# Optimization experiments

Measured on AMD Instinct MI355X. Metric: run time of the kernel, lower is better.

The kernel has to match this reference:

```python
import jax, jax.numpy as jnp
import numpy as np

ALPHA = 0.5
SIGMA = 0.5
EPS = 1e-7

def setup_inputs() -> dict:
    key = jax.random.key(0)
    k1, k2, k3, k4 = jax.random.split(key, 4)
    n, T = 8192, 256
    return {
        "hazards": jax.random.normal(k1, (n, T), dtype=jnp.float32),
        "duration": jax.random.randint(k2, (n,), 0, T, dtype=jnp.int32),
        "event": jax.random.randint(k3, (n,), 0, 2, dtype=jnp.int32),
        "label": jax.random.randint(k4, (n,), 0, T, dtype=jnp.int32),
    }

def _deephit_loss(hazards, duration, event, label):
    dur = duration.reshape(-1)
    ev = event.reshape(-1)
    lab = label.reshape(-1)
    evf = ev.astype(hazards.dtype)

    # pair_rank_mat: R_ij = 1{D_i=1 and (T_i < T_j or (T_i == T_j and D_j = 0))}
    rank_mat = ((ev[:, None] != 0)
                & ((dur[:, None] < dur[None, :])
                   | ((dur[:, None] == dur[None, :]) & (ev[None, :] == 0)))
                ).astype(hazards.dtype)  # [n, n]

    # nll_pmf (pad_col adds a zero column -> T+1 bins)
    phi = jnp.pad(hazards, ((0, 0), (0, 1)))            # [n, T+1]
    gamma = jnp.max(phi, axis=1)                         # [n]
    cumsum = jnp.cumsum(jnp.exp(phi - gamma[:, None]), axis=1)  # [n, T+1]
    sum_ = cumsum[:, -1]
    phi_at = jnp.take_along_axis(phi, lab[:, None], axis=1)[:, 0]
    cum_at = jnp.take_along_axis(cumsum, lab[:, None], axis=1)[:, 0]
    part1 = (phi_at - gamma) * evf
    part2 = -jnp.log(jnp.maximum(sum_, 0.0) + EPS)
    part3 = jnp.log(jnp.maximum(sum_ - cum_at, 0.0) + EPS) * (1.0 - evf)
    nll = jnp.mean(-(part1 + part2 + part3))

    # rank_loss_deephit_single
    pmf = jax.nn.softmax(phi, axis=1)                    # [n, T+1]
    cdf = jnp.cumsum(pmf, axis=1)                        # [n, T+1]
    y = jax.nn.one_hot(lab, phi.shape[1], dtype=pmf.dtype)  # [n, T+1]
    r = cdf @ y.T                                        # r_ij = F_i(T_j), [n, n]
    diag_r = jnp.diagonal(r)                             # F_j(T_j)
    r = (diag_r[None, :] - r).T                          # r_ij = F_i(T_i) - F_j(T_i)
    rank_loss = jnp.mean(rank_mat * jnp.exp(-r / SIGMA))

    return ALPHA * nll + (1.0 - ALPHA) * rank_loss

def reference(hazards, duration, event, label):
    return _deephit_loss(hazards, duration, event, label)
```

## Files before the change

kernel.cpp:

```cpp
#include <hip/hip_runtime.h>
#include <hip/hip_fp16.h>

#define TBINS 256
#define RPB   16
#define NTHR  1024
#define EPS_F 1e-7f
#define INV_SIGMA 2.0f

__global__ __launch_bounds__(NTHR) void row_kernel(
    const float* __restrict__ hz, const int* __restrict__ dur,
    const int* __restrict__ ev,  const int* __restrict__ lab,
    __half* __restrict__ WT, float* __restrict__ rowA,
    float* __restrict__ nllpart, int n)
{
    __shared__ float trs[RPB][260];
    __shared__ float nllred[RPB];

    const int wid  = threadIdx.x >> 6;
    const int lane = threadIdx.x & 63;
    const int row  = blockIdx.x * RPB + wid;
    const bool act = row < n;
    const int rrow = act ? row : 0;

    const float4 v = ((const float4*)(hz + (size_t)rrow * TBINS))[lane];

    float m = fmaxf(fmaxf(v.x, v.y), fmaxf(v.z, v.w));
    #pragma unroll
    for (int off = 32; off; off >>= 1) m = fmaxf(m, __shfl_xor(m, off));
    const float gamma = fmaxf(m, 0.0f);

    const float e0 = expf(v.x - gamma), e1 = expf(v.y - gamma);
    const float e2 = expf(v.z - gamma), e3 = expf(v.w - gamma);
    const float local = e0 + e1 + e2 + e3;

    float pre = local;
    #pragma unroll
    for (int off = 1; off < 64; off <<= 1) {
        float tv = __shfl_up(pre, off);
        if (lane >= off) pre += tv;
    }
    const float excl  = pre - local;
    const float total = __shfl(pre, 63);
    const float sum_  = total + expf(-gamma);
    const float c0 = excl + e0, c1 = c0 + e1, c2 = c1 + e2, c3 = c2 + e3;

    const int L = lab[rrow];
    const int e = ev[rrow];
    const int sel = L & 3;
    float csel = (sel == 0) ? c0 : (sel == 1) ? c1 : (sel == 2) ? c2 : c3;
    const float cum_at = __shfl(csel, L >> 2);
    const float inv = 1.0f / sum_;

    float4 w;
    w.x = expf(c0 * inv * INV_SIGMA);
    w.y = expf(c1 * inv * INV_SIGMA);
    w.z = expf(c2 * inv * INV_SIGMA);
    w.w = expf(c3 * inv * INV_SIGMA);
    *(float4*)&trs[wid][4 * lane] = w;

    if (lane == 0) {
        float nll_i = 0.f, a_i = 0.f;
        if (act) {
            const float phi_at = hz[(size_t)row * TBINS + L];
            const float evf = (float)e;
            const float p1 = (phi_at - gamma) * evf;
            const float p2 = -logf(fmaxf(sum_, 0.f) + EPS_F);
            const float p3 = logf(fmaxf(sum_ - cum_at, 0.f) + EPS_F) * (1.f - evf);
            nll_i = -(p1 + p2 + p3);
            a_i = e ? expf(-(cum_at * inv) * INV_SIGMA) : 0.f;
            rowA[row] = a_i;
        }
        nllred[wid] = nll_i;
    }
    __syncthreads();

    if (threadIdx.x == 0) {
        float s = 0.f;
        #pragma unroll
        for (int k = 0; k < RPB; ++k) s += nllred[k];
        nllpart[blockIdx.x] = s;
    }

    const int t  = threadIdx.x >> 2;
    const int j  = threadIdx.x & 3;
    const int i0 = blockIdx.x * RPB + 4 * j;
    if (i0 + 3 < n) {
        ushort4 p;
        p.x = __half_as_ushort(__float2half(trs[4 * j + 0][t]));
        p.y = __half_as_ushort(__float2half(trs[4 * j + 1][t]));
        p.z = __half_as_ushort(__float2half(trs[4 * j + 2][t]));
        p.w = __half_as_ushort(__float2half(trs[4 * j + 3][t]));
        *(ushort4*)&WT[(size_t)t * n + i0] = p;
    }
}

__global__ __launch_bounds__(NTHR) void agg_kernel(
    const __half* __restrict__ WT, const int* __restrict__ dur,
    const int* __restrict__ ev, float* __restrict__ B, int n)
{
    __shared__ float bins[512];

    const int t   = blockIdx.x;
    const int tid = threadIdx.x;

    if (tid < 512) bins[tid] = 0.f;
    __syncthreads();

    const __half* w = WT + (size_t)t * n;
    const int i0 = tid * 8;
    if (i0 + 7 < n) {
        const ushort4 ha = *(const ushort4*)&w[i0];
        const ushort4 hb = *(const ushort4*)&w[i0 + 4];
        const int4 da = *(const int4*)&dur[i0];
        const int4 db = *(const int4*)&dur[i0 + 4];
        const int4 ea = *(const int4*)&ev[i0];
        const int4 eb = *(const int4*)&ev[i0 + 4];
        atomicAdd(&bins[da.x + (ea.x << 8)], __half2float(__ushort_as_half(ha.x)));
        atomicAdd(&bins[da.y + (ea.y << 8)], __half2float(__ushort_as_half(ha.y)));
        atomicAdd(&bins[da.z + (ea.z << 8)], __half2float(__ushort_as_half(ha.z)));
        atomicAdd(&bins[da.w + (ea.w << 8)], __half2float(__ushort_as_half(ha.w)));
        atomicAdd(&bins[db.x + (eb.x << 8)], __half2float(__ushort_as_half(hb.x)));
        atomicAdd(&bins[db.y + (eb.y << 8)], __half2float(__ushort_as_half(hb.y)));
        atomicAdd(&bins[db.z + (eb.z << 8)], __half2float(__ushort_as_half(hb.z)));
        atomicAdd(&bins[db.w + (eb.w << 8)], __half2float(__ushort_as_half(hb.w)));
    }
    __syncthreads();

    if (tid < 64) {
        const int d0 = tid * 4;
        const float g0 = bins[d0 + 0] + bins[d0 + 256];
        const float g1 = bins[d0 + 1] + bins[d0 + 257];
        const float g2 = bins[d0 + 2] + bins[d0 + 258];
        const float g3 = bins[d0 + 3] + bins[d0 + 259];
        const float c0 = g0, c1 = c0 + g1, c2 = c1 + g2, c3 = c2 + g3;
        float pre = c3;
        #pragma unroll
        for (int off = 1; off < 64; off <<= 1) {
            float tv = __shfl_up(pre, off);
            if (tid >= off) pre += tv;
        }
        const float excl  = pre - c3;
        const float tot   = __shfl(pre, 63);
        float4 ob;
        ob.x = (tot - (excl + c0)) + bins[d0 + 0];
        ob.y = (tot - (excl + c1)) + bins[d0 + 1];
        ob.z = (tot - (excl + c2)) + bins[d0 + 2];
        ob.w = (tot - (excl + c3)) + bins[d0 + 3];
        *(float4*)&B[t * TBINS + d0] = ob;
    }
}

__global__ __launch_bounds__(NTHR) void rank_final_kernel(
    const int* __restrict__ dur, const int* __restrict__ lab,
    const float* __restrict__ rowA, const float* __restrict__ B,
    const float* __restrict__ nllpart, float* __restrict__ out,
    int n, int nblk)
{
    const int tid  = threadIdx.x;
    const int wid  = tid >> 6;
    const int lane = tid & 63;
    __shared__ float rs[16], ss[16];

    float r = 0.f;
    for (int i = tid; i < n; i += NTHR) {
        const float a = rowA[i];
        if (a != 0.f) r += a * B[lab[i] * TBINS + dur[i]];
    }
    float s = (tid < nblk) ? nllpart[tid] : 0.f;

    #pragma unroll
    for (int off = 32; off; off >>= 1) {
        r += __shfl_xor(r, off);
        s += __shfl_xor(s, off);
    }
    if (lane == 0) { rs[wid] = r; ss[wid] = s; }
    __syncthreads();
    if (tid == 0) {
        float R = 0.f, S = 0.f;
        #pragma unroll
        for (int k = 0; k < 16; ++k) { R += rs[k]; S += ss[k]; }
        const double nll = (double)S / (double)n;
        const double rl  = (double)R / ((double)n * (double)n);
        out[0] = (float)(0.5 * nll + 0.5 * rl);
    }
}

extern "C" void kernel_launch(void* const* d_in, const int* in_sizes, int n_in,
                              void* d_out, int out_size, void* d_ws, size_t ws_size,
                              hipStream_t stream) {
    const float* hz  = (const float*)d_in[0];
    const int*   dur = (const int*)d_in[1];
    const int*   ev  = (const int*)d_in[2];
    const int*   lab = (const int*)d_in[3];
    float* out = (float*)d_out;

    const int n = in_sizes[1];
    const int nblk = (n + RPB - 1) / RPB;

    __half* WT     = (__half*)d_ws;
    float*  B      = (float*)(WT + (size_t)TBINS * n);
    float*  rowA   = B + TBINS * TBINS;
    float*  nllpart= rowA + n;

    row_kernel<<<nblk, NTHR, 0, stream>>>(hz, dur, ev, lab, WT, rowA, nllpart, n);
    agg_kernel<<<TBINS, NTHR, 0, stream>>>(WT, dur, ev, B, n);
    rank_final_kernel<<<1, NTHR, 0, stream>>>(dur, lab, rowA, B, nllpart, out, n, nblk);
}
```

Before: 89.84 us.

## Fuse rank aggregation and final reduction into histogram kernel with last-block finish

The separate single-block final kernel is folded into the histogram kernel. Each block computes its own B row in shared memory and sums contributions from rows whose label matches its bin, then a global atomic counter lets the last block finish the reduction. The histogram is split into per-wave copies to reduce shared atomic contention, and the row kernel now handles two rows per wave. This removes a launch and the serial single-block pass, in exchange for global atomics, an order-dependent float sum, and a threadfence handshake.

```diff
diff --git a/kernel.cpp b/kernel.cpp
--- a/kernel.cpp
+++ b/kernel.cpp
@@ -2,136 +2,168 @@
 #include <hip/hip_fp16.h>
 
 #define TBINS 256
-#define RPB   16
+#define RPB   32
 #define NTHR  1024
 #define EPS_F 1e-7f
 #define INV_SIGMA 2.0f
 
 __global__ __launch_bounds__(NTHR) void row_kernel(
-    const float* __restrict__ hz, const int* __restrict__ dur,
-    const int* __restrict__ ev,  const int* __restrict__ lab,
+    const float* __restrict__ hz, const int* __restrict__ ev,
+    const int* __restrict__ lab,
     __half* __restrict__ WT, float* __restrict__ rowA,
-    float* __restrict__ nllpart, int n)
+    float* __restrict__ nllpart, float* __restrict__ accR, int* __restrict__ done,
+    int n)
 {
-    __shared__ float trs[RPB][260];
+    __shared__ float trs[RPB][261];
     __shared__ float nllred[RPB];
 
-    const int wid  = threadIdx.x >> 6;
-    const int lane = threadIdx.x & 63;
-    const int row  = blockIdx.x * RPB + wid;
-    const bool act = row < n;
-    const int rrow = act ? row : 0;
-
-    const float4 v = ((const float4*)(hz + (size_t)rrow * TBINS))[lane];
-
-    float m = fmaxf(fmaxf(v.x, v.y), fmaxf(v.z, v.w));
+    const int tid  = threadIdx.x;
+    const int wid  = tid >> 6;
+    const int lane = tid & 63;
+
+    if (blockIdx.x == 0 && tid == 0) { *accR = 0.f; *done = 0; }
+
     #pragma unroll
-    for (int off = 32; off; off >>= 1) m = fmaxf(m, __shfl_xor(m, off));
-    const float gamma = fmaxf(m, 0.0f);
-
-    const float e0 = expf(v.x - gamma), e1 = expf(v.y - gamma);
-    const float e2 = expf(v.z - gamma), e3 = expf(v.w - gamma);
-    const float local = e0 + e1 + e2 + e3;
-
-    float pre = local;
-    #pragma unroll
-    for (int off = 1; off < 64; off <<= 1) {
-        float tv = __shfl_up(pre, off);
-        if (lane >= off) pre += tv;
-    }
-    const float excl  = pre - local;
-    const float total = __shfl(pre, 63);
-    const float sum_  = total + expf(-gamma);
-    const float c0 = excl + e0, c1 = c0 + e1, c2 = c1 + e2, c3 = c2 + e3;
-
-    const int L = lab[rrow];
-    const int e = ev[rrow];
-    const int sel = L & 3;
-    float csel = (sel == 0) ? c0 : (sel == 1) ? c1 : (sel == 2) ? c2 : c3;
-    const float cum_at = __shfl(csel, L >> 2);
-    const float inv = 1.0f / sum_;
-
-    float4 w;
-    w.x = expf(c0 * inv * INV_SIGMA);
-    w.y = expf(c1 * inv * INV_SIGMA);
-    w.z = expf(c2 * inv * INV_SIGMA);
-    w.w = expf(c3 * inv * INV_SIGMA);
-    *(float4*)&trs[wid][4 * lane] = w;
-
-    if (lane == 0) {
-        float nll_i = 0.f, a_i = 0.f;
-        if (act) {
-            const float phi_at = hz[(size_t)row * TBINS + L];
-            const float evf = (float)e;
-            const float p1 = (phi_at - gamma) * evf;
-            const float p2 = -logf(fmaxf(sum_, 0.f) + EPS_F);
-            const float p3 = logf(fmaxf(sum_ - cum_at, 0.f) + EPS_F) * (1.f - evf);
-            nll_i = -(p1 + p2 + p3);
-            a_i = e ? expf(-(cum_at * inv) * INV_SIGMA) : 0.f;
-            rowA[row] = a_i;
-        }
-        nllred[wid] = nll_i;
-    }
-    __syncthreads();
-
-    if (threadIdx.x == 0) {
+    for (int r = 0; r < 2; ++r) {
+        const int lrow = wid * 2 + r;
+        const int row  = blockIdx.x * RPB + lrow;
+        const bool act = row < n;
+        const int rrow = act ? row : 0;
+
+        const float4 v = ((const float4*)(hz + (size_t)rrow * TBINS))[lane];
+
+        float m = fmaxf(fmaxf(v.x, v.y), fmaxf(v.z, v.w));
+        #pragma unroll
+        for (int off = 32; off; off >>= 1) m = fmaxf(m, __shfl_xor(m, off));
+        const float gamma = fmaxf(m, 0.0f);
+
+        const float e0 = expf(v.x - gamma), e1 = expf(v.y - gamma);
+        const float e2 = expf(v.z - gamma), e3 = expf(v.w - gamma);
+        const float local = e0 + e1 + e2 + e3;
+
+        float pre = local;
+        #pragma unroll
+        for (int off = 1; off < 64; off <<= 1) {
+            float tv = __shfl_up(pre, off);
+            if (lane >= off) pre += tv;
+        }
+        const float excl  = pre - local;
+        const float total = __shfl(pre, 63);
+        const float sum_  = total + expf(-gamma);
+        const float c0 = excl + e0, c1 = c0 + e1, c2 = c1 + e2, c3 = c2 + e3;
+
+        const int L = lab[rrow];
+        const int e = ev[rrow];
+        const int sel = L & 3;
+        float csel = (sel == 0) ? c0 : (sel == 1) ? c1 : (sel == 2) ? c2 : c3;
+        const float cum_at = __shfl(csel, L >> 2);
+        const float inv = 1.0f / sum_;
+
+        float4 w;
+        w.x = expf(c0 * inv * INV_SIGMA);
+        w.y = expf(c1 * inv * INV_SIGMA);
+        w.z = expf(c2 * inv * INV_SIGMA);
+        w.w = expf(c3 * inv * INV_SIGMA);
+        *(float4*)&trs[lrow][4 * lane] = w;
+
+        if (lane == 0) {
+            float nll_i = 0.f, a_i = 0.f;
+            if (act) {
+                const float phi_at = hz[(size_t)row * TBINS + L];
+                const float evf = (float)e;
+                const float p1 = (phi_at - gamma) * evf;
+                const float p2 = -logf(fmaxf(sum_, 0.f) + EPS_F);
+                const float p3 = logf(fmaxf(sum_ - cum_at, 0.f) + EPS_F) * (1.f - evf);
+                nll_i = -(p1 + p2 + p3);
+                a_i = e ? expf(-(cum_at * inv) * INV_SIGMA) : 0.f;
+                rowA[row] = a_i;
+            }
+            nllred[lrow] = nll_i;
+        }
+    }
+    __syncthreads();
+
+    if (tid == 0) {
         float s = 0.f;
         #pragma unroll
         for (int k = 0; k < RPB; ++k) s += nllred[k];
         nllpart[blockIdx.x] = s;
     }
 
-    const int t  = threadIdx.x >> 2;
-    const int j  = threadIdx.x & 3;
-    const int i0 = blockIdx.x * RPB + 4 * j;
-    if (i0 + 3 < n) {
-        ushort4 p;
-        p.x = __half_as_ushort(__float2half(trs[4 * j + 0][t]));
-        p.y = __half_as_ushort(__float2half(trs[4 * j + 1][t]));
-        p.z = __half_as_ushort(__float2half(trs[4 * j + 2][t]));
-        p.w = __half_as_ushort(__float2half(trs[4 * j + 3][t]));
-        *(ushort4*)&WT[(size_t)t * n + i0] = p;
+    #pragma unroll
+    for (int k = 0; k < 2; ++k) {
+        const int t = (tid >> 3) + 128 * k;
+        const int j = tid & 7;
+        const int i0 = blockIdx.x * RPB + 4 * j;
+        if (i0 + 3 < n) {
+            ushort4 p;
+            p.x = __half_as_ushort(__float2half(trs[4 * j + 0][t]));
+            p.y = __half_as_ushort(__float2half(trs[4 * j + 1][t]));
+            p.z = __half_as_ushort(__float2half(trs[4 * j + 2][t]));
+            p.w = __half_as_ushort(__float2half(trs[4 * j + 3][t]));
+            *(ushort4*)&WT[(size_t)t * n + i0] = p;
+        }
     }
 }
 
-__global__ __launch_bounds__(NTHR) void agg_kernel(
+__global__ __launch_bounds__(NTHR) void agg_rank_kernel(
     const __half* __restrict__ WT, const int* __restrict__ dur,
-    const int* __restrict__ ev, float* __restrict__ B, int n)
+    const int* __restrict__ ev, const int* __restrict__ lab,
+    const float* __restrict__ rowA, const float* __restrict__ nllpart,
+    float* __restrict__ accR, int* __restrict__ done,
+    float* __restrict__ out, int n, int nblk1)
 {
-    __shared__ float bins[512];
-
-    const int t   = blockIdx.x;
-    const int tid = threadIdx.x;
-
-    if (tid < 512) bins[tid] = 0.f;
-    __syncthreads();
-
-    const __half* w = WT + (size_t)t * n;
-    const int i0 = tid * 8;
-    if (i0 + 7 < n) {
-        const ushort4 ha = *(const ushort4*)&w[i0];
-        const ushort4 hb = *(const ushort4*)&w[i0 + 4];
-        const int4 da = *(const int4*)&dur[i0];
-        const int4 db = *(const int4*)&dur[i0 + 4];
-        const int4 ea = *(const int4*)&ev[i0];
-        const int4 eb = *(const int4*)&ev[i0 + 4];
-        atomicAdd(&bins[da.x + (ea.x << 8)], __half2float(__ushort_as_half(ha.x)));
-        atomicAdd(&bins[da.y + (ea.y << 8)], __half2float(__ushort_as_half(ha.y)));
-        atomicAdd(&bins[da.z + (ea.z << 8)], __half2float(__ushort_as_half(ha.z)));
-        atomicAdd(&bins[da.w + (ea.w << 8)], __half2float(__ushort_as_half(ha.w)));
-        atomicAdd(&bins[db.x + (eb.x << 8)], __half2float(__ushort_as_half(hb.x)));
-        atomicAdd(&bins[db.y + (eb.y << 8)], __half2float(__ushort_as_half(hb.y)));
-        atomicAdd(&bins[db.z + (eb.z << 8)], __half2float(__ushort_as_half(hb.z)));
-        atomicAdd(&bins[db.w + (eb.w << 8)], __half2float(__ushort_as_half(hb.w)));
+    __shared__ float hist[16][512];
+    __shared__ float comb[512];
+    __shared__ float Brow[TBINS];
+    __shared__ float red[16];
+    __shared__ int lastflag;
+
+    const int t    = blockIdx.x;
+    const int tid  = threadIdx.x;
+    const int wid  = tid >> 6;
+    const int lane = tid & 63;
+
+    for (int i = tid; i < 16 * 512; i += NTHR) ((float*)hist)[i] = 0.f;
+    __syncthreads();
+
+    {
+        const __half* w = WT + (size_t)t * n;
+        const int i0 = tid * 8;
+        if (i0 + 7 < n) {
+            const ushort4 ha = *(const ushort4*)&w[i0];
+            const ushort4 hb = *(const ushort4*)&w[i0 + 4];
+            const int4 da = *(const int4*)&dur[i0];
+            const int4 db = *(const int4*)&dur[i0 + 4];
+            const int4 ea = *(const int4*)&ev[i0];
+            const int4 eb = *(const int4*)&ev[i0 + 4];
+            float* hb_ = hist[wid];
+            atomicAdd(&hb_[da.x + (ea.x << 8)], __half2float(__ushort_as_half(ha.x)));
+            atomicAdd(&hb_[da.y + (ea.y << 8)], __half2float(__ushort_as_half(ha.y)));
+            atomicAdd(&hb_[da.z + (ea.z << 8)], __half2float(__ushort_as_half(ha.z)));
+            atomicAdd(&hb_[da.w + (ea.w << 8)], __half2float(__ushort_as_half(ha.w)));
+            atomicAdd(&hb_[db.x + (eb.x << 8)], __half2float(__ushort_as_half(hb.x)));
+            atomicAdd(&hb_[db.y + (eb.y << 8)], __half2float(__ushort_as_half(hb.y)));
+            atomicAdd(&hb_[db.z + (eb.z << 8)], __half2float(__ushort_as_half(hb.z)));
+            atomicAdd(&hb_[db.w + (eb.w << 8)], __half2float(__ushort_as_half(hb.w)));
+        }
+    }
+    __syncthreads();
+
+    if (tid < 512) {
+        float s = 0.f;
+        #pragma unroll
+        for (int k = 0; k < 16; ++k) s += hist[k][tid];
+        comb[tid] = s;
     }
     __syncthreads();
 
     if (tid < 64) {
         const int d0 = tid * 4;
-        const float g0 = bins[d0 + 0] + bins[d0 + 256];
-        const float g1 = bins[d0 + 1] + bins[d0 + 257];
-        const float g2 = bins[d0 + 2] + bins[d0 + 258];
-        const float g3 = bins[d0 + 3] + bins[d0 + 259];
+        const float g0 = comb[d0 + 0] + comb[d0 + 256];
+        const float g1 = comb[d0 + 1] + comb[d0 + 257];
+        const float g2 = comb[d0 + 2] + comb[d0 + 258];
+        const float g3 = comb[d0 + 3] + comb[d0 + 259];
         const float c0 = g0, c1 = c0 + g1, c2 = c1 + g2, c3 = c2 + g3;
         float pre = c3;
         #pragma unroll
@@ -139,49 +171,63 @@
             float tv = __shfl_up(pre, off);
             if (tid >= off) pre += tv;
         }
-        const float excl  = pre - c3;
-        const float tot   = __shfl(pre, 63);
-        float4 ob;
-        ob.x = (tot - (excl + c0)) + bins[d0 + 0];
-        ob.y = (tot - (excl + c1)) + bins[d0 + 1];
-        ob.z = (tot - (excl + c2)) + bins[d0 + 2];
-        ob.w = (tot - (excl + c3)) + bins[d0 + 3];
-        *(float4*)&B[t * TBINS + d0] = ob;
-    }
-}
-
-__global__ __launch_bounds__(NTHR) void rank_final_kernel(
-    const int* __restrict__ dur, const int* __restrict__ lab,
-    const float* __restrict__ rowA, const float* __restrict__ B,
-    const float* __restrict__ nllpart, float* __restrict__ out,
-    int n, int nblk)
-{
-    const int tid  = threadIdx.x;
-    const int wid  = tid >> 6;
-    const int lane = tid & 63;
-    __shared__ float rs[16], ss[16];
-
-    float r = 0.f;
-    for (int i = tid; i < n; i += NTHR) {
-        const float a = rowA[i];
-        if (a != 0.f) r += a * B[lab[i] * TBINS + dur[i]];
-    }
-    float s = (tid < nblk) ? nllpart[tid] : 0.f;
-
+        const float excl = pre - c3;
+        const float tot  = __shfl(pre, 63);
+        Brow[d0 + 0] = (tot - (excl + c0)) + comb[d0 + 0];
+        Brow[d0 + 1] = (tot - (excl + c1)) + comb[d0 + 1];
+        Brow[d0 + 2] = (tot - (excl + c2)) + comb[d0 + 2];
+        Brow[d0 + 3] = (tot - (excl + c3)) + comb[d0 + 3];
+    }
+    __syncthreads();
+
+    float val = 0.f;
+    {
+        const int i0 = tid * 8;
+        if (i0 + 7 < n) {
+            const int4 la = *(const int4*)&lab[i0];
+            const int4 lb = *(const int4*)&lab[i0 + 4];
+            const int ls[8] = { la.x, la.y, la.z, la.w, lb.x, lb.y, lb.z, lb.w };
+            #pragma unroll
+            for (int k = 0; k < 8; ++k) {
+                if (ls[k] == t) {
+                    const float a = rowA[i0 + k];
+                    if (a != 0.f) val += a * Brow[dur[i0 + k]];
+                }
+            }
+        }
+    }
     #pragma unroll
-    for (int off = 32; off; off >>= 1) {
-        r += __shfl_xor(r, off);
-        s += __shfl_xor(s, off);
-    }
-    if (lane == 0) { rs[wid] = r; ss[wid] = s; }
-    __syncthreads();
+    for (int off = 32; off; off >>= 1) val += __shfl_xor(val, off);
+    if (lane == 0) red[wid] = val;
+    __syncthreads();
+
     if (tid == 0) {
-        float R = 0.f, S = 0.f;
-        #pragma unroll
-        for (int k = 0; k < 16; ++k) { R += rs[k]; S += ss[k]; }
-        const double nll = (double)S / (double)n;
-        const double rl  = (double)R / ((double)n * (double)n);
-        out[0] = (float)(0.5 * nll + 0.5 * rl);
+        float s = 0.f;
+        #pragma unroll
+        for (int k = 0; k < 16; ++k) s += red[k];
+        atomicAdd(accR, s);
+        __threadfence();
+        const int old = atomicAdd(done, 1);
+        lastflag = (old == (int)gridDim.x - 1) ? 1 : 0;
+    }
+    __syncthreads();
+
+    if (lastflag) {
+        float s = (tid < nblk1) ? nllpart[tid] : 0.f;
+        #pragma unroll
+        for (int off = 32; off; off >>= 1) s += __shfl_xor(s, off);
+        if (lane == 0) red[wid] = s;
+        __syncthreads();
+        if (tid == 0) {
+            float S = 0.f;
+            #pragma unroll
+            for (int k = 0; k < 16; ++k) S += red[k];
+            __threadfence();
+            const float R = atomicAdd(accR, 0.0f);
+            const double nll = (double)S / (double)n;
+            const double rl  = (double)R / ((double)n * (double)n);
+            out[0] = (float)(0.5 * nll + 0.5 * rl);
+        }
     }
 }
 
@@ -195,14 +241,15 @@
     float* out = (float*)d_out;
 
     const int n = in_sizes[1];
-    const int nblk = (n + RPB - 1) / RPB;
-
-    __half* WT     = (__half*)d_ws;
-    float*  B      = (float*)(WT + (size_t)TBINS * n);
-    float*  rowA   = B + TBINS * TBINS;
-    float*  nllpart= rowA + n;
-
-    row_kernel<<<nblk, NTHR, 0, stream>>>(hz, dur, ev, lab, WT, rowA, nllpart, n);
-    agg_kernel<<<TBINS, NTHR, 0, stream>>>(WT, dur, ev, B, n);
-    rank_final_kernel<<<1, NTHR, 0, stream>>>(dur, lab, rowA, B, nllpart, out, n, nblk);
+    const int nblk1 = (n + RPB - 1) / RPB;
+
+    __half* WT      = (__half*)d_ws;
+    float*  rowA    = (float*)(WT + (size_t)TBINS * n);
+    float*  nllpart = rowA + n;
+    float*  accR    = nllpart + nblk1;
+    int*    done    = (int*)(accR + 1);
+
+    row_kernel<<<nblk1, NTHR, 0, stream>>>(hz, ev, lab, WT, rowA, nllpart, accR, done, n);
+    agg_rank_kernel<<<TBINS, NTHR, 0, stream>>>(WT, dur, ev, lab, rowA, nllpart,
+                                                accR, done, out, n, nblk1);
 }
```

New measurement: 88.33 us. Within noise of the previous version (-1.7%).
